# Performance work log

Measured on AMD Instinct MI355X. Metric: run time of the kernel, lower is better.

The kernel has to match this reference:

```python
import jax, jax.numpy as jnp
import numpy as np

B_, L_, D_ = 2, 1024, 2048
E_, N_, R_, K_ = 4096, 16, 128, 4
EPS = 1e-5


def setup_inputs() -> dict:
    key = jax.random.key(0)
    ks = jax.random.split(key, 12)
    s = lambda i, shape, scale=0.02: jax.random.normal(ks[i], shape, jnp.float32) * scale
    # dt bias init as in the module: inv_dt = dt + log(-expm1(-dt)), dt ~ logU[1e-3, 0.1]
    dt = jnp.exp(jax.random.uniform(ks[10], (E_,)) * (np.log(0.1) - np.log(0.001)) + np.log(0.001))
    inv_dt = dt + jnp.log(-jnp.expm1(-dt))
    return {
        'resid': jax.random.normal(ks[0], (B_, L_, D_), jnp.float32),
        'norm_w': jnp.ones((D_,), jnp.float32),
        'skip_w': s(1, (E_, D_)),
        'in_w': s(2, (E_, D_)),
        'conv_w': s(3, (E_, K_), 0.2),
        'conv_b': jnp.zeros((E_,), jnp.float32),
        'wd1': s(4, (R_, E_)),
        'wd2': s(5, (E_, R_), R_ ** -0.5),
        'wd2_b': inv_dt,
        'wB': s(6, (N_, E_)),
        'wC': s(7, (N_, E_)),
        'A_log': jnp.log(jnp.broadcast_to(jnp.arange(1, N_ + 1, dtype=jnp.float32), (E_, N_))),
        'W_D': jnp.ones((E_,), jnp.float32),
        'out_w': s(8, (D_, E_)),
    }


def _forward(resid, norm_w, skip_w, in_w, conv_w, conv_b, wd1, wd2, wd2_b,
             wB, wC, A_log, W_D, out_w):
    B, L, D = resid.shape
    E, K = conv_w.shape
    N = A_log.shape[1]
    # RMSNorm
    rn = resid * jax.lax.rsqrt(jnp.mean(resid * resid, -1, keepdims=True) + EPS) * norm_w
    skip = rn @ skip_w.T                       # [B,L,E] gate branch (z)
    x_in = rn @ in_w.T                         # [B,L,E]
    # depthwise causal conv1d (pad left K-1, truncate to L), then SiLU
    xp = jnp.pad(x_in, ((0, 0), (K - 1, 0), (0, 0)))
    conv = conv_b + sum(xp[:, k:k + L, :] * conv_w[:, k] for k in range(K))
    x = jax.nn.silu(conv)                      # [B,L,E] ssm input
    # low-rank delta, input-dependent B/C
    delta = jax.nn.softplus((x @ wd1.T) @ wd2.T + wd2_b)   # [B,L,E]
    A = -jnp.exp(A_log)                        # [E,N]
    Bm = x @ wB.T                              # [B,L,N]
    Cm = x @ wC.T                              # [B,L,N]

    def step(h, inp):
        d_l, b_l, c_l, x_l = inp               # [B,E],[B,N],[B,N],[B,E]
        h = jnp.exp(d_l[:, :, None] * A) * h + (d_l * x_l)[:, :, None] * b_l[:, None, :]
        y_l = jnp.einsum('ben,bn->be', h, c_l)
        return h, y_l

    h0 = jnp.zeros((B, E, N), resid.dtype)
    xs = (delta.transpose(1, 0, 2), Bm.transpose(1, 0, 2),
          Cm.transpose(1, 0, 2), x.transpose(1, 0, 2))
    _, ys = jax.lax.scan(step, h0, xs)         # ys: [L,B,E]
    y = ys.transpose(1, 0, 2) + x * W_D        # skip connection via D
    y = y * jax.nn.silu(skip)                  # gating
    return resid + y @ out_w.T                 # out_proj + residual


def reference(resid, norm_w, skip_w, in_w, conv_w, conv_b, wd1, wd2, wd2_b,
              wB, wC, A_log, W_D, out_w):
    return _forward(resid, norm_w, skip_w, in_w, conv_w, conv_b, wd1, wd2,
                    wd2_b, wB, wC, A_log, W_D, out_w)
```

## Files before the change

kernel.cpp:

```cpp
#include <hip/hip_runtime.h>
#include <stdint.h>

#define NB 2
#define NL 1024
#define ND 2048
#define NE 4096
#define NN 16
#define NR 128
#define NKC 4
#define NBL (NB*NL)
#define EPSV 1e-5f
#define SEG_T 256
#define SCAN_T 64

typedef __attribute__((ext_vector_type(4))) float f32x4;
typedef __attribute__((ext_vector_type(8))) short short8;
typedef __attribute__((ext_vector_type(8))) unsigned short ushort8;
typedef __attribute__((ext_vector_type(4))) unsigned short ushort4_t;

__device__ __forceinline__ unsigned short f2bf(float f) {
  union { float f; unsigned u; } v; v.f = f;
  unsigned r = v.u + 0x7FFFu + ((v.u >> 16) & 1u);
  return (unsigned short)(r >> 16);
}

__device__ __forceinline__ float bf2f(unsigned short u) {
  union { unsigned u; float f; } v; v.u = (unsigned)u << 16; return v.f;
}

__device__ __forceinline__ void load_lds16(const void* g, void* l) {
  __builtin_amdgcn_global_load_lds((const __attribute__((address_space(1))) void*)g,
                                   (__attribute__((address_space(3))) void*)l,
                                   16, 0, 0);
}

template<int CTRL>
__device__ __forceinline__ float dpp_mov(float v) {
  return __int_as_float(__builtin_amdgcn_update_dpp(
      0, __float_as_int(v), CTRL, 0xF, 0xF, true));
}

__global__ void rmsnorm_kernel(const float* __restrict__ resid,
                               const float* __restrict__ nw,
                               unsigned short* __restrict__ rn) {
  int row = blockIdx.x;
  int tid = threadIdx.x;
  const float* r = resid + (size_t)row * ND;
  f32x4 v0 = *(const f32x4*)(r + tid * 8);
  f32x4 v1 = *(const f32x4*)(r + tid * 8 + 4);
  float vals[8];
#pragma unroll
  for (int i = 0; i < 4; ++i) { vals[i] = v0[i]; vals[4 + i] = v1[i]; }
  float ss = 0.f;
#pragma unroll
  for (int i = 0; i < 8; ++i) ss += vals[i] * vals[i];
  for (int o = 32; o > 0; o >>= 1) ss += __shfl_down(ss, o);
  __shared__ float ps[4];
  if ((tid & 63) == 0) ps[tid >> 6] = ss;
  __syncthreads();
  float tot = ps[0] + ps[1] + ps[2] + ps[3];
  float scale = rsqrtf(tot / (float)ND + EPSV);
  ushort8 o8;
#pragma unroll
  for (int i = 0; i < 8; ++i) o8[i] = f2bf(vals[i] * scale * nw[tid * 8 + i]);
  *(ushort8*)(rn + (size_t)row * ND + tid * 8) = o8;
}

__global__ void cast_bf16_kernel(const float* __restrict__ in,
                                 unsigned short* __restrict__ out, int n8) {
  int i = blockIdx.x * blockDim.x + threadIdx.x;
  if (i >= n8) return;
  f32x4 a = *(const f32x4*)(in + (size_t)i * 8);
  f32x4 b = *(const f32x4*)(in + (size_t)i * 8 + 4);
  ushort8 o;
#pragma unroll
  for (int j = 0; j < 4; ++j) { o[j] = f2bf(a[j]); o[4 + j] = f2bf(b[j]); }
  *(ushort8*)(out + (size_t)i * 8) = o;
}

__global__ void build_wcat_kernel(const float* __restrict__ wd1,
                                  const float* __restrict__ wB,
                                  const float* __restrict__ wC,
                                  unsigned short* __restrict__ out) {
  int i = blockIdx.x * blockDim.x + threadIdx.x;
  if (i >= 256 * NE / 8) return;
  int col8 = i & (NE / 8 - 1);
  int row = i >> 9;
  const float* src = nullptr; int srow = 0;
  if (row < 128)      { src = wd1; srow = row; }
  else if (row < 144) { src = wB;  srow = row - 128; }
  else if (row < 160) { src = wC;  srow = row - 144; }
  ushort8 o;
  if (src) {
    f32x4 a = *(const f32x4*)(src + (size_t)srow * NE + col8 * 8);
    f32x4 b = *(const f32x4*)(src + (size_t)srow * NE + col8 * 8 + 4);
#pragma unroll
    for (int j = 0; j < 4; ++j) { o[j] = f2bf(a[j]); o[4 + j] = f2bf(b[j]); }
  } else {
#pragma unroll
    for (int j = 0; j < 8; ++j) o[j] = 0;
  }
  *(ushort8*)(out + (size_t)row * NE + col8 * 8) = o;
}

__global__ __launch_bounds__(512, 2)
void gemm256_fused(const unsigned short* __restrict__ A,
                   const unsigned short* __restrict__ B,
                   float* __restrict__ Gout,
                   unsigned short* __restrict__ Xout) {
  const int K = 2048, NH = K / 32;
  __shared__ unsigned short Asl[4][8192];
  __shared__ unsigned short Bsl[4][8192];
  int tid = threadIdx.x;
  int w = tid >> 6, lane = tid & 63;
  int wm = w >> 2, wn = w & 3;
  int lr = lane & 15, kg8 = (lane >> 4) * 8;
  int m0 = blockIdx.y * 256, n0 = blockIdx.x * 256;

  const unsigned short* ga = A + (size_t)(m0 + (tid >> 2)) * K + (tid & 3) * 8;
  const unsigned short* gb = B + (size_t)(n0 + (tid >> 2)) * K + (tid & 3) * 8;
  char* ldsA0 = (char*)&Asl[0][0] + w * 1024;
  char* ldsB0 = (char*)&Bsl[0][0] + w * 1024;

  auto stageA = [&](int h) {
    int slot = h & 3, k0 = h * 32;
    load_lds16(ga + k0, ldsA0 + slot * 16384);
    load_lds16(ga + k0 + (size_t)128 * K, ldsA0 + slot * 16384 + 8192);
  };
  auto stageB = [&](int h) {
    int slot = h & 3, k0 = h * 32;
    load_lds16(gb + k0, ldsB0 + slot * 16384);
    load_lds16(gb + k0 + (size_t)128 * K, ldsB0 + slot * 16384 + 8192);
  };

  f32x4 acc[8][4];
#pragma unroll
  for (int i = 0; i < 8; ++i)
#pragma unroll
    for (int j = 0; j < 4; ++j) acc[i][j] = (f32x4){0.f, 0.f, 0.f, 0.f};

  stageA(0); stageB(0); stageA(1); stageB(1); stageA(2); stageB(2);
  asm volatile("s_waitcnt vmcnt(8)" ::: "memory");
  __builtin_amdgcn_s_barrier();

  for (int h = 0; h < NH; ++h) {
    int slot = h & 3;
    const unsigned short* As_ = &Asl[slot][0];
    const unsigned short* Bs_ = &Bsl[slot][0];
    int arow = wm * 128 + lr;
    int brow = wn * 64 + lr;
    short8 a[8], b[4];
#pragma unroll
    for (int i = 0; i < 4; ++i)
      a[i] = *(const short8*)&As_[(arow + i * 16) * 32 + kg8];
#pragma unroll
    for (int j = 0; j < 4; ++j)
      b[j] = *(const short8*)&Bs_[(brow + j * 16) * 32 + kg8];
    if (h + 3 < NH) stageA(h + 3);
    __builtin_amdgcn_s_barrier();
    __builtin_amdgcn_s_setprio(1);
#pragma unroll
    for (int i = 0; i < 4; ++i)
#pragma unroll
      for (int j = 0; j < 4; ++j)
        acc[i][j] = __builtin_amdgcn_mfma_f32_16x16x32_bf16(a[i], b[j], acc[i][j], 0, 0, 0);
    __builtin_amdgcn_s_setprio(0);
    __builtin_amdgcn_s_barrier();
#pragma unroll
    for (int i = 0; i < 4; ++i)
      a[4 + i] = *(const short8*)&As_[(arow + (4 + i) * 16) * 32 + kg8];
    if (h + 3 < NH) stageB(h + 3);
    __builtin_amdgcn_s_barrier();
    __builtin_amdgcn_s_setprio(1);
#pragma unroll
    for (int i = 0; i < 4; ++i)
#pragma unroll
      for (int j = 0; j < 4; ++j)
        acc[4 + i][j] = __builtin_amdgcn_mfma_f32_16x16x32_bf16(a[4 + i], b[j], acc[4 + i][j], 0, 0, 0);
    __builtin_amdgcn_s_setprio(0);
    if (h < NH - 3)       { asm volatile("s_waitcnt vmcnt(8)" ::: "memory"); }
    else if (h == NH - 3) { asm volatile("s_waitcnt vmcnt(4)" ::: "memory"); }
    else if (h == NH - 2) { asm volatile("s_waitcnt vmcnt(0)" ::: "memory"); }
    __builtin_amdgcn_s_barrier();
  }

  int rbase = m0 + wm * 128 + (lane >> 4) * 4;
  int cbase = n0 + wn * 64 + (lane & 15);
  bool isg = (n0 < 4096);
#pragma unroll
  for (int mf = 0; mf < 8; ++mf) {
#pragma unroll
    for (int nf = 0; nf < 4; ++nf) {
      int col = cbase + nf * 16;
#pragma unroll
      for (int rr = 0; rr < 4; ++rr) {
        int row = rbase + mf * 16 + rr;
        float v = acc[mf][nf][rr];
        if (isg) Gout[(size_t)row * 4096 + col] = v / (1.f + __expf(-v));
        else     Xout[(size_t)row * 4096 + (col - 4096)] = f2bf(v);
      }
    }
  }
}

template<int MODE>
__global__ __launch_bounds__(256)
void gemm_bt(const unsigned short* __restrict__ A,
             const unsigned short* __restrict__ B,
             float* __restrict__ C,
             int M, int N, int K, int ksteps_per_z,
             const float* __restrict__ bias,
             const float* __restrict__ add) {
  __shared__ unsigned short As[128 * 32];
  __shared__ unsigned short Bs[128 * 32];
  int tid = threadIdx.x;
  int w = tid >> 6, lane = tid & 63;
  int m0 = blockIdx.y * 128, n0 = blockIdx.x * 128;
  int kz0 = blockIdx.z * ksteps_per_z * 32;
  if (MODE == 0) C += (size_t)blockIdx.z * M * N;

  f32x4 zero = {0.f, 0.f, 0.f, 0.f};
  f32x4 acc[4][4];
#pragma unroll
  for (int i = 0; i < 4; ++i)
#pragma unroll
    for (int j = 0; j < 4; ++j) acc[i][j] = zero;

  int wm = w >> 1, wn = w & 1;
  int lr = lane & 15, kg = lane >> 4;

  int fe0 = (w)*512 + lane * 8;
  int fe1 = (4 + w) * 512 + lane * 8;
  int r0 = fe0 >> 5, c0 = fe0 & 31;
  int r1 = fe1 >> 5, c1 = fe1 & 31;
  const unsigned short* Ag0 = A + (size_t)(m0 + r0) * K + c0;
  const unsigned short* Ag1 = A + (size_t)(m0 + r1) * K + c1;
  const unsigned short* Bg0 = B + (size_t)(n0 + r0) * K + c0;
  const unsigned short* Bg1 = B + (size_t)(n0 + r1) * K + c1;
  unsigned short* Al0 = As + (w) * 512;
  unsigned short* Al1 = As + (4 + w) * 512;
  unsigned short* Bl0 = Bs + (w) * 512;
  unsigned short* Bl1 = Bs + (4 + w) * 512;

  for (int ks = 0; ks < ksteps_per_z; ++ks) {
    int kk = kz0 + ks * 32;
    __syncthreads();
    load_lds16(Ag0 + kk, Al0);
    load_lds16(Ag1 + kk, Al1);
    load_lds16(Bg0 + kk, Bl0);
    load_lds16(Bg1 + kk, Bl1);
    asm volatile("s_waitcnt vmcnt(0)" ::: "memory");
    __syncthreads();
    short8 a[4], b[4];
#pragma unroll
    for (int i = 0; i < 4; ++i)
      a[i] = *(const short8*)&As[(wm * 64 + i * 16 + lr) * 32 + kg * 8];
#pragma unroll
    for (int j = 0; j < 4; ++j)
      b[j] = *(const short8*)&Bs[(wn * 64 + j * 16 + lr) * 32 + kg * 8];
#pragma unroll
    for (int i = 0; i < 4; ++i)
#pragma unroll
      for (int j = 0; j < 4; ++j)
        acc[i][j] = __builtin_amdgcn_mfma_f32_16x16x32_bf16(a[i], b[j], acc[i][j], 0, 0, 0);
  }

#pragma unroll
  for (int i = 0; i < 4; ++i) {
#pragma unroll
    for (int j = 0; j < 4; ++j) {
      int rbase = m0 + wm * 64 + i * 16 + kg * 4;
      int col = n0 + wn * 64 + j * 16 + lr;
#pragma unroll
      for (int r = 0; r < 4; ++r) {
        float v = acc[i][j][r];
        size_t idx = (size_t)(rbase + r) * N + col;
        if (MODE == 0) {
          C[idx] = v;
        } else if (MODE == 1) {
          float t = v + bias[col];
          ((unsigned short*)C)[idx] = f2bf((t > 20.f) ? t : log1pf(__expf(t)));
        } else {
          C[idx] = v + add[idx];
        }
      }
    }
  }
}

__global__ void conv_silu_kernel(const unsigned short* __restrict__ xin,
                                 const float* __restrict__ cw,
                                 const float* __restrict__ cb,
                                 unsigned short* __restrict__ xbf) {
  size_t idx = (size_t)blockIdx.x * blockDim.x + threadIdx.x;
  if (idx >= (size_t)NB * NL * NE) return;
  int e = (int)(idx & (NE - 1));
  int r = (int)(idx >> 12);
  int l = r & (NL - 1);
  float acc = cb[e];
#pragma unroll
  for (int k = 0; k < NKC; ++k) {
    int ls = l - 3 + k;
    if (ls >= 0) acc += bf2f(xin[(size_t)(r - 3 + k) * NE + e]) * cw[e * 4 + k];
  }
  float s = acc / (1.f + __expf(-acc));
  xbf[idx] = f2bf(s);
}

__global__ void reduce_tcat_kernel(const float* __restrict__ part,
                                   unsigned short* __restrict__ tbf,
                                   float* __restrict__ bc) {
  int idx = blockIdx.x * blockDim.x + threadIdx.x;
  if (idx >= NBL * 160) return;
  int m = idx / 160, c = idx - m * 160;
  float s = 0.f;
#pragma unroll
  for (int z = 0; z < 8; ++z) s += part[(size_t)z * NBL * 256 + (size_t)m * 256 + c];
  if (c < 128) tbf[m * 128 + c] = f2bf(s);
  else if (c < 144) bc[m * 32 + (c - 128)] = s;
  else bc[m * 32 + 16 + (c - 144)] = s;
}

__global__ __launch_bounds__(256)
void scan1_kernel(const unsigned short* __restrict__ delta_bf,
                  const unsigned short* __restrict__ x_bf,
                  const float* __restrict__ bc,
                  const float* __restrict__ gf,
                  const float* __restrict__ A_log,
                  const float* __restrict__ W_D,
                  unsigned short* __restrict__ yg,
                  float* __restrict__ fin,
                  float* __restrict__ dtot) {
  __shared__ unsigned short dxl[2][SCAN_T][2][16];
  __shared__ float gl[2][SCAN_T][16];
  __shared__ float BCl[2][SCAN_T][32];
  __shared__ float yl2[SCAN_T][16][2];
  __shared__ float wdl[16];
  int tid = threadIdx.x;
  int n = tid & 15, el = tid >> 4;
  int w = tid >> 6, lane = tid & 63;
  int e0 = blockIdx.x * 16;
  int b = blockIdx.y >> 2, seg = blockIdx.y & 3;
  int e = e0 + el;
  float A2 = -__expf(A_log[e * 16 + n]) * 1.44269504f;
  if (tid < 16) wdl[tid] = W_D[e0 + tid];
  float h = 0.f, cum = 0.f;

  const unsigned short* gdl = delta_bf + (size_t)b * NL * NE + e0;
  const unsigned short* gx  = x_bf + (size_t)b * NL * NE + e0;
  const float* gg  = gf + (size_t)b * NL * 4096 + e0;
  const float* gBC = bc + (size_t)b * NL * 32;

  const unsigned short* dxsrc = ((lane >> 1) & 1) ? gx : gdl;
  int dxrow = w * 16 + (lane >> 2);
  int dxcol = (lane & 1) * 8;
  int grow = w * 16 + (lane >> 2);
  int gcol = (lane & 3) * 4;
  int bcrow = lane >> 3;
  int bccol = (lane & 7) * 4;

  auto stage = [&](int buf, int c) {
    int l0 = seg * SEG_T + c * SCAN_T;
    load_lds16(dxsrc + (size_t)(l0 + dxrow) * NE + dxcol, &dxl[buf][w * 16][0][0]);
    if (seg == 0)
      load_lds16(gg + (size_t)(l0 + grow) * 4096 + gcol, &gl[buf][w * 16][0]);
    load_lds16(gBC + (size_t)(l0 + w * 16 + bcrow) * 32 + bccol, &BCl[buf][w * 16][0]);
    load_lds16(gBC + (size_t)(l0 + w * 16 + 8 + bcrow) * 32 + bccol, &BCl[buf][w * 16 + 8][0]);
  };

  stage(0, 0);
  const int nch = SEG_T / SCAN_T;
  for (int c = 0; c < nch; ++c) {
    int cur = c & 1;
    if (c + 1 < nch) {
      stage(cur ^ 1, c + 1);
      if (seg == 0) { asm volatile("s_waitcnt vmcnt(4)" ::: "memory"); }
      else          { asm volatile("s_waitcnt vmcnt(3)" ::: "memory"); }
    } else {
      asm volatile("s_waitcnt vmcnt(0)" ::: "memory");
    }
    __syncthreads();
    const unsigned short (*dxc)[2][16] = dxl[cur];
    const float (*BCc)[32] = BCl[cur];
#pragma unroll 8
    for (int t = 0; t < SCAN_T; ++t) {
      float dc = bf2f(dxc[t][0][el]);
      float xc = bf2f(dxc[t][1][el]);
      float Bc = BCc[t][n];
      float Cc = BCc[t][16 + n];
      cum += dc;
      float a = dc * A2, ed;
      asm("v_exp_f32 %0, %1" : "=v"(ed) : "v"(a));
      h = ed * h + (dc * xc) * Bc;
      float p = h * Cc;
      p += dpp_mov<0xB1>(p);
      p += dpp_mov<0x4E>(p);
      p += dpp_mov<0x141>(p);
      if ((n & 7) == 0) yl2[t][el][n >> 3] = p;
    }
    __syncthreads();
    {
      int t = tid >> 2, part = tid & 3;
      int l0 = seg * SEG_T + c * SCAN_T;
      ushort4_t o;
#pragma unroll
      for (int j = 0; j < 4; ++j) {
        int ee = part * 4 + j;
        float xv = bf2f(dxc[t][1][ee]);
        float y = yl2[t][ee][0] + yl2[t][ee][1] + xv * wdl[ee];
        if (seg == 0) y *= gl[cur][t][ee];
        o[j] = f2bf(y);
      }
      *(ushort4_t*)(yg + (size_t)(b * NL + l0 + t) * NE + e0 + part * 4) = o;
    }
    __syncthreads();
  }
  fin[(size_t)((seg * 2 + b) * 4096 + e) * 16 + n] = h;
  if (n == 0) dtot[(size_t)(seg * 2 + b) * 4096 + e] = cum;
}

__global__ __launch_bounds__(256)
void scan2_kernel(const unsigned short* __restrict__ delta_bf,
                  unsigned short* __restrict__ yg,
                  const float* __restrict__ bc,
                  const float* __restrict__ gf,
                  const float* __restrict__ A_log,
                  const float* __restrict__ fin,
                  const float* __restrict__ dtot) {
  __shared__ unsigned short dl[2][SCAN_T][16];
  __shared__ unsigned short ypl[2][SCAN_T][16];
  __shared__ float Cl[2][SCAN_T][16];
  __shared__ float gl2[2][SCAN_T][16];
  __shared__ float ycl[SCAN_T][16][2];
  int tid = threadIdx.x;
  int n = tid & 15, el = tid >> 4;
  int w = tid >> 6, lane = tid & 63;
  int e0 = blockIdx.x * 16;
  int b = blockIdx.y / 3, seg = 1 + blockIdx.y % 3;
  int e = e0 + el;
  float A2 = -__expf(A_log[e * 16 + n]) * 1.44269504f;
  float h = fin[(size_t)(b * 4096 + e) * 16 + n];
  for (int s2 = 1; s2 < seg; ++s2) {
    float dt = dtot[(size_t)(s2 * 2 + b) * 4096 + e];
    float a = A2 * dt, pw;
    asm("v_exp_f32 %0, %1" : "=v"(pw) : "v"(a));
    h = fin[(size_t)((s2 * 2 + b) * 4096 + e) * 16 + n] + pw * h;
  }

  const unsigned short* gd = delta_bf + (size_t)b * NL * NE + e0;
  unsigned short* gy = yg + (size_t)b * NL * NE + e0;
  const float* gg  = gf + (size_t)b * NL * 4096 + e0;
  const float* gBC = bc + (size_t)b * NL * 32;

  int crow = w * 16 + (lane >> 2);
  int ccol = 16 + (lane & 3) * 4;
  int grow = w * 16 + (lane >> 2);
  int gcol = (lane & 3) * 4;
  int dyrow = (w & 1) * 32 + (lane >> 1);
  int dycol = (lane & 1) * 8;

  auto stage = [&](int buf, int c) {
    int l0 = seg * SEG_T + c * SCAN_T;
    load_lds16(gBC + (size_t)(l0 + crow) * 32 + ccol, &Cl[buf][w * 16][0]);
    load_lds16(gg + (size_t)(l0 + grow) * 4096 + gcol, &gl2[buf][w * 16][0]);
    if (w < 2) load_lds16(gd + (size_t)(l0 + dyrow) * NE + dycol, &dl[buf][(w & 1) * 32][0]);
    else       load_lds16(gy + (size_t)(l0 + dyrow) * NE + dycol, &ypl[buf][(w & 1) * 32][0]);
  };

  stage(0, 0);
  float cum = 0.f;
  const int nch = SEG_T / SCAN_T;
  for (int c = 0; c < nch; ++c) {
    int cur = c & 1;
    if (c + 1 < nch) {
      stage(cur ^ 1, c + 1);
      asm volatile("s_waitcnt vmcnt(3)" ::: "memory");
    } else {
      asm volatile("s_waitcnt vmcnt(0)" ::: "memory");
    }
    __syncthreads();
    const unsigned short (*dc_)[16] = dl[cur];
    const float (*Cc_)[16] = Cl[cur];
#pragma unroll 8
    for (int t = 0; t < SCAN_T; ++t) {
      float dcv = bf2f(dc_[t][el]);
      cum += dcv;
      float a = A2 * cum, pw;
      asm("v_exp_f32 %0, %1" : "=v"(pw) : "v"(a));
      float p = (pw * h) * Cc_[t][n];
      p += dpp_mov<0xB1>(p);
      p += dpp_mov<0x4E>(p);
      p += dpp_mov<0x141>(p);
      if ((n & 7) == 0) ycl[t][el][n >> 3] = p;
    }
    __syncthreads();
    {
      int t = tid >> 2, part = tid & 3;
      int l0 = seg * SEG_T + c * SCAN_T;
      ushort4_t o;
#pragma unroll
      for (int j = 0; j < 4; ++j) {
        int ee = part * 4 + j;
        float y = ycl[t][ee][0] + ycl[t][ee][1] + bf2f(ypl[cur][t][ee]);
        o[j] = f2bf(y * gl2[cur][t][ee]);
      }
      *(ushort4_t*)(gy + (size_t)(l0 + t) * NE + part * 4) = o;
    }
    __syncthreads();
  }
}

extern "C" void kernel_launch(void* const* d_in, const int* in_sizes, int n_in,
                              void* d_out, int out_size, void* d_ws, size_t ws_size,
                              hipStream_t stream) {
  const float* resid  = (const float*)d_in[0];
  const float* norm_w = (const float*)d_in[1];
  const float* skip_w = (const float*)d_in[2];
  const float* in_w   = (const float*)d_in[3];
  const float* conv_w = (const float*)d_in[4];
  const float* conv_b = (const float*)d_in[5];
  const float* wd1    = (const float*)d_in[6];
  const float* wd2    = (const float*)d_in[7];
  const float* wd2_b  = (const float*)d_in[8];
  const float* wB     = (const float*)d_in[9];
  const float* wC     = (const float*)d_in[10];
  const float* A_log  = (const float*)d_in[11];
  const float* W_D    = (const float*)d_in[12];
  const float* out_w  = (const float*)d_in[13];
  float* out = (float*)d_out;

  char* ws = (char*)d_ws;
  size_t off = 0;
  auto alloc = [&](size_t bytes) -> void* {
    void* p = ws + off;
    off += (bytes + 255) & ~(size_t)255;
    return p;
  };
  unsigned short* rn_bf      = (unsigned short*)alloc((size_t)NBL * ND * 2);
  unsigned short* wskipin_bf = (unsigned short*)alloc((size_t)2 * NE * ND * 2);
  unsigned short* wout_bf    = (unsigned short*)alloc((size_t)ND * NE * 2);
  unsigned short* wd2_bf     = (unsigned short*)alloc((size_t)NE * NR * 2);
  unsigned short* wcat_bf    = (unsigned short*)alloc((size_t)256 * NE * 2);
  float* g_f                 = (float*)alloc((size_t)NBL * NE * 4);
  unsigned short* xin_bf     = (unsigned short*)alloc((size_t)NBL * NE * 2);
  unsigned short* x_bf       = (unsigned short*)alloc((size_t)NBL * NE * 2);
  float* part_f              = (float*)alloc((size_t)8 * NBL * 256 * 4);
  unsigned short* t_bf       = (unsigned short*)alloc((size_t)NBL * NR * 2);
  float* bc_f                = (float*)alloc((size_t)NBL * 32 * 4);
  unsigned short* yg_bf      = (unsigned short*)alloc((size_t)NBL * NE * 2);
  float* fin_f               = (float*)alloc((size_t)4 * NB * NE * 16 * 4);
  float* dtot_f              = (float*)alloc((size_t)4 * NB * NE * 4);
  unsigned short* delta_bf = wskipin_bf;
  (void)ws_size; (void)in_sizes; (void)n_in; (void)out_size;

  rmsnorm_kernel<<<dim3(NBL), dim3(256), 0, stream>>>(resid, norm_w, rn_bf);

  cast_bf16_kernel<<<dim3((NE * ND / 8 + 255) / 256), dim3(256), 0, stream>>>(skip_w, wskipin_bf, NE * ND / 8);
  cast_bf16_kernel<<<dim3((NE * ND / 8 + 255) / 256), dim3(256), 0, stream>>>(in_w, wskipin_bf + (size_t)NE * ND, NE * ND / 8);
  cast_bf16_kernel<<<dim3((ND * NE / 8 + 255) / 256), dim3(256), 0, stream>>>(out_w, wout_bf, ND * NE / 8);
  cast_bf16_kernel<<<dim3((NE * NR / 8 + 255) / 256), dim3(256), 0, stream>>>(wd2, wd2_bf, NE * NR / 8);
  build_wcat_kernel<<<dim3(256 * NE / 8 / 256), dim3(256), 0, stream>>>(wd1, wB, wC, wcat_bf);

  gemm256_fused<<<dim3(8192 / 256, NBL / 256), dim3(512), 0, stream>>>(
      rn_bf, wskipin_bf, g_f, xin_bf);

  conv_silu_kernel<<<dim3((int)(((size_t)NB * NL * NE) / 256)), dim3(256), 0, stream>>>(
      xin_bf, conv_w, conv_b, x_bf);

  gemm_bt<0><<<dim3(256 / 128, NBL / 128, 8), dim3(256), 0, stream>>>(
      x_bf, wcat_bf, part_f, NBL, 256, NE, (NE / 32) / 8, nullptr, nullptr);
  reduce_tcat_kernel<<<dim3((NBL * 160 + 255) / 256), dim3(256), 0, stream>>>(
      part_f, t_bf, bc_f);

  gemm_bt<1><<<dim3(NE / 128, NBL / 128, 1), dim3(256), 0, stream>>>(
      t_bf, wd2_bf, (float*)delta_bf, NBL, NE, NR, NR / 32, wd2_b, nullptr);

  scan1_kernel<<<dim3(NE / 16, NB * 4), dim3(256), 0, stream>>>(
      delta_bf, x_bf, bc_f, g_f, A_log, W_D, yg_bf, fin_f, dtot_f);
  scan2_kernel<<<dim3(NE / 16, NB * 3), dim3(256), 0, stream>>>(
      delta_bf, yg_bf, bc_f, g_f, A_log, fin_f, dtot_f);

  gemm_bt<2><<<dim3(ND / 128, NBL / 128, 1), dim3(256), 0, stream>>>(
      yg_bf, wout_bf, out, NBL, ND, NE, NE / 32, nullptr, resid);
}
```

Measured before the change: 463.2 us.

## Pipeline generic GEMM K-loop with 4-slot LDS ring and prefetch depth three

Replaces the single-buffered LDS tile load in gemm_bt with a four-slot ring buffer that issues global-to-LDS loads three K-steps ahead. Partial vmcnt waits replace the full wait so MFMA work on the current slot overlaps with in-flight loads. It also raises wave priority around the MFMA block. LDS use grows fourfold to 64KB per block, which can lower occupancy. Correctness depends on the vmcnt counts matching the four loads issued per stage.

```diff
diff --git a/kernel.cpp b/kernel.cpp
--- a/kernel.cpp
+++ b/kernel.cpp
@@ -211,58 +211,69 @@
              int M, int N, int K, int ksteps_per_z,
              const float* __restrict__ bias,
              const float* __restrict__ add) {
-  __shared__ unsigned short As[128 * 32];
-  __shared__ unsigned short Bs[128 * 32];
+  __shared__ unsigned short As[4][128 * 32];
+  __shared__ unsigned short Bs[4][128 * 32];
   int tid = threadIdx.x;
   int w = tid >> 6, lane = tid & 63;
   int m0 = blockIdx.y * 128, n0 = blockIdx.x * 128;
   int kz0 = blockIdx.z * ksteps_per_z * 32;
   if (MODE == 0) C += (size_t)blockIdx.z * M * N;
-
-  f32x4 zero = {0.f, 0.f, 0.f, 0.f};
+  const int NH = ksteps_per_z;
+
   f32x4 acc[4][4];
 #pragma unroll
   for (int i = 0; i < 4; ++i)
 #pragma unroll
-    for (int j = 0; j < 4; ++j) acc[i][j] = zero;
+    for (int j = 0; j < 4; ++j) acc[i][j] = (f32x4){0.f, 0.f, 0.f, 0.f};
 
   int wm = w >> 1, wn = w & 1;
   int lr = lane & 15, kg = lane >> 4;
 
-  int fe0 = (w)*512 + lane * 8;
+  int fe0 = (w) * 512 + lane * 8;
   int fe1 = (4 + w) * 512 + lane * 8;
   int r0 = fe0 >> 5, c0 = fe0 & 31;
   int r1 = fe1 >> 5, c1 = fe1 & 31;
-  const unsigned short* Ag0 = A + (size_t)(m0 + r0) * K + c0;
-  const unsigned short* Ag1 = A + (size_t)(m0 + r1) * K + c1;
-  const unsigned short* Bg0 = B + (size_t)(n0 + r0) * K + c0;
-  const unsigned short* Bg1 = B + (size_t)(n0 + r1) * K + c1;
-  unsigned short* Al0 = As + (w) * 512;
-  unsigned short* Al1 = As + (4 + w) * 512;
-  unsigned short* Bl0 = Bs + (w) * 512;
-  unsigned short* Bl1 = Bs + (4 + w) * 512;
-
-  for (int ks = 0; ks < ksteps_per_z; ++ks) {
-    int kk = kz0 + ks * 32;
-    __syncthreads();
-    load_lds16(Ag0 + kk, Al0);
-    load_lds16(Ag1 + kk, Al1);
-    load_lds16(Bg0 + kk, Bl0);
-    load_lds16(Bg1 + kk, Bl1);
-    asm volatile("s_waitcnt vmcnt(0)" ::: "memory");
-    __syncthreads();
+  const unsigned short* Ag0 = A + (size_t)(m0 + r0) * K + c0 + kz0;
+  const unsigned short* Ag1 = A + (size_t)(m0 + r1) * K + c1 + kz0;
+  const unsigned short* Bg0 = B + (size_t)(n0 + r0) * K + c0 + kz0;
+  const unsigned short* Bg1 = B + (size_t)(n0 + r1) * K + c1 + kz0;
+
+  auto stage = [&](int h) {
+    int slot = h & 3, kk = h * 32;
+    load_lds16(Ag0 + kk, &As[slot][(w) * 512]);
+    load_lds16(Ag1 + kk, &As[slot][(4 + w) * 512]);
+    load_lds16(Bg0 + kk, &Bs[slot][(w) * 512]);
+    load_lds16(Bg1 + kk, &Bs[slot][(4 + w) * 512]);
+  };
+
+  stage(0);
+  if (NH > 1) stage(1);
+  if (NH > 2) stage(2);
+
+  for (int h = 0; h < NH; ++h) {
+    int slot = h & 3;
+    __builtin_amdgcn_s_barrier();
+    if (h + 3 < NH) stage(h + 3);
+    int rem = NH - 1 - h; if (rem > 3) rem = 3;
+    if (rem == 3)      { asm volatile("s_waitcnt vmcnt(12)" ::: "memory"); }
+    else if (rem == 2) { asm volatile("s_waitcnt vmcnt(8)"  ::: "memory"); }
+    else if (rem == 1) { asm volatile("s_waitcnt vmcnt(4)"  ::: "memory"); }
+    else               { asm volatile("s_waitcnt vmcnt(0)"  ::: "memory"); }
+    __builtin_amdgcn_s_barrier();
     short8 a[4], b[4];
 #pragma unroll
     for (int i = 0; i < 4; ++i)
-      a[i] = *(const short8*)&As[(wm * 64 + i * 16 + lr) * 32 + kg * 8];
+      a[i] = *(const short8*)&As[slot][(wm * 64 + i * 16 + lr) * 32 + kg * 8];
 #pragma unroll
     for (int j = 0; j < 4; ++j)
-      b[j] = *(const short8*)&Bs[(wn * 64 + j * 16 + lr) * 32 + kg * 8];
+      b[j] = *(const short8*)&Bs[slot][(wn * 64 + j * 16 + lr) * 32 + kg * 8];
+    __builtin_amdgcn_s_setprio(1);
 #pragma unroll
     for (int i = 0; i < 4; ++i)
 #pragma unroll
       for (int j = 0; j < 4; ++j)
         acc[i][j] = __builtin_amdgcn_mfma_f32_16x16x32_bf16(a[i], b[j], acc[i][j], 0, 0, 0);
+    __builtin_amdgcn_s_setprio(0);
   }
 
 #pragma unroll
```

Result: faster. 448.9 us (-3.1%).
